# Performance work log

Measured on AMD Instinct MI355X. Metric: run time of the kernel, lower is better.

The kernel has to match this reference:

```python
import jax, jax.numpy as jnp
import numpy as np

NEG_NUM = -10000.0


def setup_inputs() -> dict:
    key = jax.random.key(0)
    k1, k2, k3 = jax.random.split(key, 3)
    B, S, T, D = 8, 4096, 512, 1024
    ctx = jax.random.normal(k1, (B, S, D), dtype=jnp.float32)
    query = jax.random.normal(k2, (B, T, D), dtype=jnp.float32)
    mask = jax.random.randint(k3, (B, S), 0, 2, dtype=jnp.int32)
    return {"ctx": ctx, "query": query, "mask": mask}


def reference(ctx, query, mask):
    # ctx: [B, S, D], query: [B, T, D], mask: [B, S] (0 = masked)
    D = query.shape[-1]
    denom = jnp.asarray(np.sqrt(D), dtype=ctx.dtype)
    # scores[b, t, s] = sum_d query[b, t, d] * ctx[b, s, d]
    scores = jnp.einsum("btd,bsd->bts", query, ctx) / denom
    # apply mask per source position (broadcast over target dim)
    scores = jnp.where(mask[:, None, :] == 0, NEG_NUM, scores)
    p_ctx = jax.nn.softmax(scores, axis=-1)  # [B, T, S]
    expected_ctx = jnp.einsum("bts,bsd->btd", p_ctx, ctx)  # [B, T, D]
    return expected_ctx, p_ctx
```

## Files before the change

### kernel.cpp

```cpp
#include <hip/hip_runtime.h>

#define BB 8
#define SS 4096
#define TT 512
#define DD 1024

typedef __attribute__((ext_vector_type(8))) short bf16x8;
typedef __attribute__((ext_vector_type(4))) short bf16x4;
typedef __attribute__((ext_vector_type(4))) float f32x4;

#define GLOAD_LDS16(gp, lp)                                            \
  __builtin_amdgcn_global_load_lds(                                    \
      (const __attribute__((address_space(1))) void*)(gp),             \
      (__attribute__((address_space(3))) void*)(lp), 16, 0, 0)

__device__ inline unsigned short f2bf(float f) {
  unsigned int u = __float_as_uint(f);
  u += 0x7FFFu + ((u >> 16) & 1u);
  return (unsigned short)(u >> 16);
}
__device__ inline void pack16(const float* __restrict__ src, short* __restrict__ dst) {
  f32x4 f0 = *(const f32x4*)(src + 0);
  f32x4 f1 = *(const f32x4*)(src + 4);
  f32x4 f2 = *(const f32x4*)(src + 8);
  f32x4 f3 = *(const f32x4*)(src + 12);
  bf16x8 b0, b1;
  b0[0] = (short)f2bf(f0.x); b0[1] = (short)f2bf(f0.y);
  b0[2] = (short)f2bf(f0.z); b0[3] = (short)f2bf(f0.w);
  b0[4] = (short)f2bf(f1.x); b0[5] = (short)f2bf(f1.y);
  b0[6] = (short)f2bf(f1.z); b0[7] = (short)f2bf(f1.w);
  b1[0] = (short)f2bf(f2.x); b1[1] = (short)f2bf(f2.y);
  b1[2] = (short)f2bf(f2.z); b1[3] = (short)f2bf(f2.w);
  b1[4] = (short)f2bf(f3.x); b1[5] = (short)f2bf(f3.y);
  b1[6] = (short)f2bf(f3.z); b1[7] = (short)f2bf(f3.w);
  *(bf16x8*)(dst + 0) = b0;
  *(bf16x8*)(dst + 8) = b1;
}

#define WS_NEED ((size_t)168 << 20)
#define OFF_QB  ((size_t)0)
#define OFF_CB  ((size_t)8 << 20)
#define OFF_CT  ((size_t)72 << 20)
#define OFF_PB  ((size_t)136 << 20)
#define OFF_PART ((size_t)0)

__global__ __launch_bounds__(256) void prep_q_kernel(const float* __restrict__ q,
                                                     short* __restrict__ qb) {
  const size_t idx = ((size_t)blockIdx.x * 256 + threadIdx.x) * 16;
  pack16(q + idx, qb + idx);
}

__global__ __launch_bounds__(256) void prep_c_kernel(const float* __restrict__ c,
                                                     short* __restrict__ cb,
                                                     short* __restrict__ ct) {
  const int b  = blockIdx.z;
  const int s0 = blockIdx.y * 64;
  const int d0 = blockIdx.x * 64;
  const float* C = c + (size_t)b * SS * DD;
  __shared__ float Tt[64][65];

  const int tid = threadIdx.x;
#pragma unroll
  for (int h = 0; h < 4; ++h) {
    const int sl = (tid >> 4) + h * 16;
    const int dl = (tid & 15) * 4;
    f32x4 v = *(const f32x4*)(C + (size_t)(s0 + sl) * DD + d0 + dl);
    *(f32x4*)&Tt[sl][dl] = v;
    bf16x4 o;
    o[0] = (short)f2bf(v.x); o[1] = (short)f2bf(v.y);
    o[2] = (short)f2bf(v.z); o[3] = (short)f2bf(v.w);
    *(bf16x4*)(cb + (size_t)b * SS * DD + (size_t)(s0 + sl) * DD + d0 + dl) = o;
  }
  __syncthreads();
#pragma unroll
  for (int g = 0; g < 2; ++g) {
    const int dl = (tid >> 3) + g * 32;
    const int sb = (tid & 7) * 8;
    bf16x8 o;
#pragma unroll
    for (int j = 0; j < 8; ++j) o[j] = (short)f2bf(Tt[sb + j][dl]);
    *(bf16x8*)(ct + (size_t)b * DD * SS + (size_t)(d0 + dl) * SS + s0 + sb) = o;
  }
}


__global__ __launch_bounds__(256) void qk_kernel_f(const short* __restrict__ qb,
                                                   const short* __restrict__ cb,
                                                   const int* __restrict__ mask,
                                                   float* __restrict__ p) {
  const int b  = blockIdx.z;
  const int m0 = blockIdx.y * 128;
  const int n0 = blockIdx.x * 128;
  const short* A  = qb + (size_t)b * TT * DD;
  const short* Bt = cb + (size_t)b * SS * DD;

  __shared__ alignas(16) short As[128 * 64];
  __shared__ alignas(16) short Bs[128 * 64];

  const int tid  = threadIdx.x;
  const int wave = tid >> 6, lane = tid & 63;
  const int quad = lane >> 4, l16 = lane & 15;
  const int wm = (wave >> 1) * 64, wn = (wave & 1) * 64;

  const int rl = lane >> 3;
  const int ck = (lane & 7) ^ (lane >> 3);
  const int x7 = l16 & 7;

  f32x4 acc[4][4];
#pragma unroll
  for (int i = 0; i < 4; ++i)
#pragma unroll
    for (int j = 0; j < 4; ++j) acc[i][j] = (f32x4){0.f, 0.f, 0.f, 0.f};

  for (int k0 = 0; k0 < DD; k0 += 64) {
    __syncthreads();
#pragma unroll
    for (int t = 0; t < 4; ++t) {
      const int rb = wave * 32 + t * 8;
      GLOAD_LDS16(A  + (size_t)(m0 + rb + rl) * DD + k0 + ck * 8, &As[rb * 64]);
      GLOAD_LDS16(Bt + (size_t)(n0 + rb + rl) * DD + k0 + ck * 8, &Bs[rb * 64]);
    }
    __syncthreads();

#pragma unroll
    for (int kk = 0; kk < 2; ++kk) {
      bf16x8 af[4], bfv[4];
#pragma unroll
      for (int i = 0; i < 4; ++i)
        af[i] = *(const bf16x8*)&As[(wm + i * 16 + l16) * 64 +
                                    (((kk * 4 + quad) ^ x7) * 8)];
#pragma unroll
      for (int j = 0; j < 4; ++j)
        bfv[j] = *(const bf16x8*)&Bs[(wn + j * 16 + l16) * 64 +
                                     (((kk * 4 + quad) ^ x7) * 8)];
#pragma unroll
      for (int i = 0; i < 4; ++i)
#pragma unroll
        for (int j = 0; j < 4; ++j)
          acc[i][j] = __builtin_amdgcn_mfma_f32_16x16x32_bf16(af[i], bfv[j],
                                                              acc[i][j], 0, 0, 0);
    }
  }

  float* P = p + (size_t)b * TT * SS;
  int mk[4];
#pragma unroll
  for (int j = 0; j < 4; ++j) mk[j] = mask[b * SS + n0 + wn + j * 16 + l16];
#pragma unroll
  for (int i = 0; i < 4; ++i)
#pragma unroll
    for (int j = 0; j < 4; ++j)
#pragma unroll
      for (int r = 0; r < 4; ++r) {
        const int row = m0 + wm + i * 16 + quad * 4 + r;
        const int col = n0 + wn + j * 16 + l16;
        const float val = (mk[j] == 0) ? -10000.0f : acc[i][j][r] * 0.03125f;
        P[(size_t)row * SS + col] = val;
      }
}

__global__ __launch_bounds__(256) void softmax_kernel_f(float* __restrict__ p,
                                                        short* __restrict__ pb) {
  const int wave = threadIdx.x >> 6, lane = threadIdx.x & 63;
  const int row = blockIdx.x * 4 + wave;
  float* pr = p + (size_t)row * SS;
  short* pbr = pb + (size_t)row * SS;

  f32x4 v[16];
  float mx = -3.0e38f;
#pragma unroll
  for (int h = 0; h < 16; ++h) {
    v[h] = *(const f32x4*)(pr + h * 256 + lane * 4);
    mx = fmaxf(mx, fmaxf(fmaxf(v[h].x, v[h].y), fmaxf(v[h].z, v[h].w)));
  }
#pragma unroll
  for (int off = 32; off > 0; off >>= 1) mx = fmaxf(mx, __shfl_xor(mx, off));

  float sum = 0.f;
#pragma unroll
  for (int h = 0; h < 16; ++h) {
    v[h].x = __expf(v[h].x - mx);
    v[h].y = __expf(v[h].y - mx);
    v[h].z = __expf(v[h].z - mx);
    v[h].w = __expf(v[h].w - mx);
    sum += (v[h].x + v[h].y) + (v[h].z + v[h].w);
  }
#pragma unroll
  for (int off = 32; off > 0; off >>= 1) sum += __shfl_xor(sum, off);
  const float inv = 1.0f / sum;

#pragma unroll
  for (int h = 0; h < 16; ++h) {
    f32x4 o;
    o.x = v[h].x * inv; o.y = v[h].y * inv;
    o.z = v[h].z * inv; o.w = v[h].w * inv;
    *(f32x4*)(pr + h * 256 + lane * 4) = o;
    bf16x4 ob;
    ob[0] = (short)f2bf(o.x); ob[1] = (short)f2bf(o.y);
    ob[2] = (short)f2bf(o.z); ob[3] = (short)f2bf(o.w);
    *(bf16x4*)(pbr + h * 256 + lane * 4) = ob;
  }
}

__global__ __launch_bounds__(256) void pv_kernel_f(const short* __restrict__ pb,
                                                   const short* __restrict__ ct,
                                                   float* __restrict__ part) {
  const int n0 = blockIdx.x * 128;
  const int m0 = blockIdx.y * 128;
  const int z  = blockIdx.z;
  const int b  = z >> 1;
  const int ks = z & 1;
  const short* A  = pb + (size_t)b * TT * SS;
  const short* Bt = ct + (size_t)b * DD * SS;

  __shared__ alignas(16) short As[128 * 64];
  __shared__ alignas(16) short Bs[128 * 64];

  const int tid  = threadIdx.x;
  const int wave = tid >> 6, lane = tid & 63;
  const int quad = lane >> 4, l16 = lane & 15;
  const int wm = (wave >> 1) * 64, wn = (wave & 1) * 64;

  const int rl = lane >> 3;
  const int ck = (lane & 7) ^ (lane >> 3);
  const int x7 = l16 & 7;

  f32x4 acc[4][4];
#pragma unroll
  for (int i = 0; i < 4; ++i)
#pragma unroll
    for (int j = 0; j < 4; ++j) acc[i][j] = (f32x4){0.f, 0.f, 0.f, 0.f};

  const int kend = ks * 2048 + 2048;
  for (int k0 = ks * 2048; k0 < kend; k0 += 64) {
    __syncthreads();
#pragma unroll
    for (int t = 0; t < 4; ++t) {
      const int rb = wave * 32 + t * 8;
      GLOAD_LDS16(A  + (size_t)(m0 + rb + rl) * SS + k0 + ck * 8, &As[rb * 64]);
      GLOAD_LDS16(Bt + (size_t)(n0 + rb + rl) * SS + k0 + ck * 8, &Bs[rb * 64]);
    }
    __syncthreads();

#pragma unroll
    for (int kk = 0; kk < 2; ++kk) {
      bf16x8 af[4], bfv[4];
#pragma unroll
      for (int i = 0; i < 4; ++i)
        af[i] = *(const bf16x8*)&As[(wm + i * 16 + l16) * 64 +
                                    (((kk * 4 + quad) ^ x7) * 8)];
#pragma unroll
      for (int j = 0; j < 4; ++j)
        bfv[j] = *(const bf16x8*)&Bs[(wn + j * 16 + l16) * 64 +
                                     (((kk * 4 + quad) ^ x7) * 8)];
#pragma unroll
      for (int i = 0; i < 4; ++i)
#pragma unroll
        for (int j = 0; j < 4; ++j)
          acc[i][j] = __builtin_amdgcn_mfma_f32_16x16x32_bf16(af[i], bfv[j],
                                                              acc[i][j], 0, 0, 0);
    }
  }

  float* E = part + (size_t)ks * BB * TT * DD + (size_t)b * TT * DD;
#pragma unroll
  for (int i = 0; i < 4; ++i)
#pragma unroll
    for (int j = 0; j < 4; ++j)
#pragma unroll
      for (int r = 0; r < 4; ++r) {
        const int row = m0 + wm + i * 16 + quad * 4 + r;
        const int col = n0 + wn + j * 16 + l16;
        E[(size_t)row * DD + col] = acc[i][j][r];
      }
}

__global__ __launch_bounds__(256) void reduce_kernel(const float* __restrict__ part,
                                                     float* __restrict__ e) {
  const size_t idx = ((size_t)blockIdx.x * 256 + threadIdx.x) * 4;
  const size_t N = (size_t)BB * TT * DD;
  f32x4 a0 = *(const f32x4*)(part + idx);
  f32x4 a1 = *(const f32x4*)(part + N + idx);
  f32x4 o;
  o.x = a0.x + a1.x;
  o.y = a0.y + a1.y;
  o.z = a0.z + a1.z;
  o.w = a0.w + a1.w;
  *(f32x4*)(e + idx) = o;
}

__global__ __launch_bounds__(256) void qk_kernel(const float* __restrict__ q,
                                                 const float* __restrict__ c,
                                                 float* __restrict__ p) {
  const int b  = blockIdx.z;
  const int m0 = blockIdx.y * 128;
  const int n0 = blockIdx.x * 128;
  const float* A  = q + (size_t)b * TT * DD;
  const float* Bt = c + (size_t)b * SS * DD;
  __shared__ alignas(16) short As[128 * 40];
  __shared__ alignas(16) short Bs[128 * 40];
  const int tid  = threadIdx.x;
  const int wave = tid >> 6, lane = tid & 63;
  const int quad = lane >> 4, l16 = lane & 15;
  const int wm = (wave >> 1) * 64, wn = (wave & 1) * 64;
  f32x4 acc[4][4];
#pragma unroll
  for (int i = 0; i < 4; ++i)
#pragma unroll
    for (int j = 0; j < 4; ++j) acc[i][j] = (f32x4){0.f, 0.f, 0.f, 0.f};
  const int ar = tid >> 1;
  const int ak = (tid & 1) * 16;
  for (int k0 = 0; k0 < DD; k0 += 32) {
    __syncthreads();
    pack16(A  + (size_t)(m0 + ar) * DD + k0 + ak, &As[ar * 40 + ak]);
    pack16(Bt + (size_t)(n0 + ar) * DD + k0 + ak, &Bs[ar * 40 + ak]);
    __syncthreads();
    bf16x8 af[4], bfv[4];
#pragma unroll
  for (int i = 0; i < 4; ++i)
      af[i] = *(const bf16x8*)&As[(wm + i * 16 + l16) * 40 + quad * 8];
#pragma unroll
    for (int j = 0; j < 4; ++j)
      bfv[j] = *(const bf16x8*)&Bs[(wn + j * 16 + l16) * 40 + quad * 8];
#pragma unroll
    for (int i = 0; i < 4; ++i)
#pragma unroll
      for (int j = 0; j < 4; ++j)
        acc[i][j] = __builtin_amdgcn_mfma_f32_16x16x32_bf16(af[i], bfv[j],
                                                            acc[i][j], 0, 0, 0);
  }
  float* P = p + (size_t)b * TT * SS;
#pragma unroll
  for (int i = 0; i < 4; ++i)
#pragma unroll
    for (int j = 0; j < 4; ++j)
#pragma unroll
      for (int r = 0; r < 4; ++r) {
        const int row = m0 + wm + i * 16 + quad * 4 + r;
        const int col = n0 + wn + j * 16 + l16;
        P[(size_t)row * SS + col] = acc[i][j][r] * 0.03125f;
      }
}

__global__ __launch_bounds__(256) void softmax_kernel(float* __restrict__ p,
                                                      const int* __restrict__ mask) {
  const int row = blockIdx.x;
  const int b   = row >> 9;
  float* pr = p + (size_t)row * SS;
  const int* mr = mask + b * SS;
  const int tid = threadIdx.x;
  const int wave = tid >> 6, lane = tid & 63;
  float v[16];
  float mx = -3.0e38f;
#pragma unroll
  for (int h = 0; h < 4; ++h) {
    const int base = tid * 4 + h * 1024;
    f32x4 s = *(const f32x4*)(pr + base);
    const int4 m4 = *(const int4*)(mr + base);
#pragma unroll
    for (int j = 0; j < 4; ++j) {
      float f = (j == 0 ? s.x : j == 1 ? s.y : j == 2 ? s.z : s.w);
      const int mk = (j == 0 ? m4.x : j == 1 ? m4.y : j == 2 ? m4.z : m4.w);
      f = fminf(fmaxf(f, -1.0e30f), 1.0e30f);
      f = (mk == 0) ? -10000.0f : f;
      v[h * 4 + j] = f;
      mx = fmaxf(mx, f);
    }
  }
#pragma unroll
  for (int off = 32; off > 0; off >>= 1) mx = fmaxf(mx, __shfl_down(mx, off));
  __shared__ float red[4];
  if (lane == 0) red[wave] = mx;
  __syncthreads();
  mx = fmaxf(fmaxf(red[0], red[1]), fmaxf(red[2], red[3]));
  __syncthreads();
  float e[16];
  float sum = 0.f;
#pragma unroll
  for (int k = 0; k < 16; ++k) { e[k] = __expf(v[k] - mx); sum += e[k]; }
#pragma unroll
  for (int off = 32; off > 0; off >>= 1) sum += __shfl_down(sum, off);
  if (lane == 0) red[wave] = sum;
  __syncthreads();
  const float inv = 1.0f / (red[0] + red[1] + red[2] + red[3]);
#pragma unroll
  for (int h = 0; h < 4; ++h) {
    const int base = tid * 4 + h * 1024;
    f32x4 o;
    o.x = e[h * 4 + 0] * inv; o.y = e[h * 4 + 1] * inv;
    o.z = e[h * 4 + 2] * inv; o.w = e[h * 4 + 3] * inv;
    *(f32x4*)(pr + base) = o;
  }
}

__global__ __launch_bounds__(256) void pv_kernel(const float* __restrict__ p,
                                                 const float* __restrict__ c,
                                                 float* __restrict__ e) {
  const int b  = blockIdx.z;
  const int m0 = blockIdx.y * 128;
  const int n0 = blockIdx.x * 128;
  const float* A  = p + (size_t)b * TT * SS;
  const float* Bm = c + (size_t)b * SS * DD;
  __shared__ alignas(16) short As[128 * 40];
  __shared__ alignas(16) short Bs[128 * 40];
  const int tid  = threadIdx.x;
  const int wave = tid >> 6, lane = tid & 63;
  const int quad = lane >> 4, l16 = lane & 15;
  const int wm = (wave >> 1) * 64, wn = (wave & 1) * 64;
  f32x4 acc[4][4];
#pragma unroll
  for (int i = 0; i < 4; ++i)
#pragma unroll
    for (int j = 0; j < 4; ++j) acc[i][j] = (f32x4){0.f, 0.f, 0.f, 0.f};
  const int ar = tid >> 1;
  const int ak = (tid & 1) * 16;
  const int kk = tid >> 3;
  const int c0 = (tid & 7) * 16;
  for (int k0 = 0; k0 < SS; k0 += 32) {
    __syncthreads();
    pack16(A + (size_t)(m0 + ar) * SS + k0 + ak, &As[ar * 40 + ak]);
    {
      const float* bp = Bm + (size_t)(k0 + kk) * DD + n0 + c0;
#pragma unroll
      for (int h = 0; h < 4; ++h) {
        f32x4 f = *(const f32x4*)(bp + h * 4);
        Bs[(c0 + h * 4 + 0) * 40 + kk] = (short)f2bf(f.x);
        Bs[(c0 + h * 4 + 1) * 40 + kk] = (short)f2bf(f.y);
        Bs[(c0 + h * 4 + 2) * 40 + kk] = (short)f2bf(f.z);
        Bs[(c0 + h * 4 + 3) * 40 + kk] = (short)f2bf(f.w);
      }
    }
    __syncthreads();
    bf16x8 af[4], bfv[4];
#pragma unroll
    for (int i = 0; i < 4; ++i)
      af[i] = *(const bf16x8*)&As[(wm + i * 16 + l16) * 40 + quad * 8];
#pragma unroll
    for (int j = 0; j < 4; ++j)
      bfv[j] = *(const bf16x8*)&Bs[(wn + j * 16 + l16) * 40 + quad * 8];
#pragma unroll
    for (int i = 0; i < 4; ++i)
#pragma unroll
      for (int j = 0; j < 4; ++j)
        acc[i][j] = __builtin_amdgcn_mfma_f32_16x16x32_bf16(af[i], bfv[j],
                                                            acc[i][j], 0, 0, 0);
  }
  float* E = e + (size_t)b * TT * DD;
#pragma unroll
  for (int i = 0; i < 4; ++i)
#pragma unroll
    for (int j = 0; j < 4; ++j)
#pragma unroll
      for (int r = 0; r < 4; ++r) {
        const int row = m0 + wm + i * 16 + quad * 4 + r;
        const int col = n0 + wn + j * 16 + l16;
        E[(size_t)row * DD + col] = acc[i][j][r];
      }
}

extern "C" void kernel_launch(void* const* d_in, const int* in_sizes, int n_in,
                              void* d_out, int out_size, void* d_ws, size_t ws_size,
                              hipStream_t stream) {
  const float* ctx   = (const float*)d_in[0];
  const float* query = (const float*)d_in[1];
  const int*   mask  = (const int*)d_in[2];

  float* expected = (float*)d_out;
  float* p        = (float*)d_out + (size_t)BB * TT * DD;

  if (ws_size >= WS_NEED) {
    char* ws = (char*)d_ws;
    short* qb = (short*)(ws + OFF_QB);
    short* cb = (short*)(ws + OFF_CB);
    short* ct = (short*)(ws + OFF_CT);
    short* pb = (short*)(ws + OFF_PB);
    float* part = (float*)(ws + OFF_PART);

    prep_q_kernel<<<dim3((BB * TT * DD) / (256 * 16)), 256, 0, stream>>>(query, qb);
    prep_c_kernel<<<dim3(DD / 64, SS / 64, BB), 256, 0, stream>>>(ctx, cb, ct);
    qk_kernel_f<<<dim3(SS / 128, TT / 128, BB), 256, 0, stream>>>(qb, cb, mask, p);
    softmax_kernel_f<<<dim3((BB * TT) / 4), 256, 0, stream>>>(p, pb);
    pv_kernel_f<<<dim3(DD / 128, TT / 128, BB * 2), 256, 0, stream>>>(pb, ct, part);
    reduce_kernel<<<dim3((BB * TT * DD) / (256 * 4)), 256, 0, stream>>>(part, expected);
  } else {
    qk_kernel<<<dim3(SS / 128, TT / 128, BB), 256, 0, stream>>>(query, ctx, p);
    softmax_kernel<<<dim3(BB * TT), 256, 0, stream>>>(p, mask);
    pv_kernel<<<dim3(DD / 128, TT / 128, BB), 256, 0, stream>>>(p, ctx, expected);
  }
}
```

Baseline: 398.9 us.

## Double-buffer LDS tiles in QK and PV GEMMs and retile context transpose

The QK and PV GEMM kernels now use two LDS buffers so the async global-to-LDS load of the next K tile is issued before computing on the current tile, leaving one barrier per iteration instead of two. The context prep kernel processes 128 source rows per block, holds all eight loads in registers before converting, and uses an XOR-swizzled float tile for the transpose instead of a padded array. The goal is to hide global load latency behind MFMA work and cut barrier stalls. The cost is doubled LDS per block (64 KB), which may reduce occupancy. The single barrier per iteration may also be insufficient to guarantee the async loads are visible before they are read.

```diff
diff --git a/kernel.cpp b/kernel.cpp
--- a/kernel.cpp
+++ b/kernel.cpp
@@ -54,32 +54,43 @@
                                                      short* __restrict__ cb,
                                                      short* __restrict__ ct) {
   const int b  = blockIdx.z;
-  const int s0 = blockIdx.y * 64;
+  const int s0 = blockIdx.y * 128;
   const int d0 = blockIdx.x * 64;
   const float* C = c + (size_t)b * SS * DD;
-  __shared__ float Tt[64][65];
+  __shared__ float T[128 * 64];
 
   const int tid = threadIdx.x;
-#pragma unroll
-  for (int h = 0; h < 4; ++h) {
-    const int sl = (tid >> 4) + h * 16;
-    const int dl = (tid & 15) * 4;
-    f32x4 v = *(const f32x4*)(C + (size_t)(s0 + sl) * DD + d0 + dl);
-    *(f32x4*)&Tt[sl][dl] = v;
+  const int r0 = tid >> 4;
+  const int cc = tid & 15;
+
+  f32x4 v[8];
+#pragma unroll
+  for (int i = 0; i < 8; ++i)
+    v[i] = *(const f32x4*)(C + (size_t)(s0 + r0 + i * 16) * DD + d0 + cc * 4);
+
+#pragma unroll
+  for (int i = 0; i < 8; ++i) {
+    const int r = r0 + i * 16;
     bf16x4 o;
-    o[0] = (short)f2bf(v.x); o[1] = (short)f2bf(v.y);
-    o[2] = (short)f2bf(v.z); o[3] = (short)f2bf(v.w);
-    *(bf16x4*)(cb + (size_t)b * SS * DD + (size_t)(s0 + sl) * DD + d0 + dl) = o;
+    o[0] = (short)f2bf(v[i].x); o[1] = (short)f2bf(v[i].y);
+    o[2] = (short)f2bf(v[i].z); o[3] = (short)f2bf(v[i].w);
+    *(bf16x4*)(cb + (size_t)b * SS * DD + (size_t)(s0 + r) * DD + d0 + cc * 4) = o;
+    *(f32x4*)&T[r * 64 + ((cc ^ (r >> 3)) & 15) * 4] = v[i];
   }
   __syncthreads();
-#pragma unroll
-  for (int g = 0; g < 2; ++g) {
-    const int dl = (tid >> 3) + g * 32;
-    const int sb = (tid & 7) * 8;
+
+  const int sc  = (tid & 15) * 8;
+  const int dr0 = tid >> 4;
+#pragma unroll
+  for (int i = 0; i < 4; ++i) {
+    const int d = dr0 + i * 16;
     bf16x8 o;
 #pragma unroll
-    for (int j = 0; j < 8; ++j) o[j] = (short)f2bf(Tt[sb + j][dl]);
-    *(bf16x8*)(ct + (size_t)b * DD * SS + (size_t)(d0 + dl) * SS + s0 + sb) = o;
+    for (int j = 0; j < 8; ++j) {
+      const int s = sc + j;
+      o[j] = (short)f2bf(T[s * 64 + (((d >> 2) ^ (s >> 3)) & 15) * 4 + (d & 3)]);
+    }
+    *(bf16x8*)(ct + (size_t)b * DD * SS + (size_t)(d0 + d) * SS + s0 + sc) = o;
   }
 }
 
@@ -94,8 +105,8 @@
   const short* A  = qb + (size_t)b * TT * DD;
   const short* Bt = cb + (size_t)b * SS * DD;
 
-  __shared__ alignas(16) short As[128 * 64];
-  __shared__ alignas(16) short Bs[128 * 64];
+  __shared__ alignas(16) short As[2][128 * 64];
+  __shared__ alignas(16) short Bs[2][128 * 64];
 
   const int tid  = threadIdx.x;
   const int wave = tid >> 6, lane = tid & 63;
@@ -112,35 +123,50 @@
 #pragma unroll
     for (int j = 0; j < 4; ++j) acc[i][j] = (f32x4){0.f, 0.f, 0.f, 0.f};
 
-  for (int k0 = 0; k0 < DD; k0 += 64) {
+#define QK_STAGE(buf, k0)                                                     \
+  {                                                                           \
+    _Pragma("unroll")                                                         \
+    for (int t = 0; t < 4; ++t) {                                             \
+      const int rb = wave * 32 + t * 8;                                       \
+      GLOAD_LDS16(A  + (size_t)(m0 + rb + rl) * DD + (k0) + ck * 8,           \
+                  &As[buf][rb * 64]);                                         \
+      GLOAD_LDS16(Bt + (size_t)(n0 + rb + rl) * DD + (k0) + ck * 8,           \
+                  &Bs[buf][rb * 64]);                                         \
+    }                                                                         \
+  }
+
+#define QK_COMPUTE(buf)                                                       \
+  {                                                                           \
+    _Pragma("unroll")                                                         \
+    for (int kk = 0; kk < 2; ++kk) {                                          \
+      bf16x8 af[4], bfv[4];                                                   \
+      _Pragma("unroll")                                                       \
+      for (int i = 0; i < 4; ++i)                                             \
+        af[i] = *(const bf16x8*)&As[buf][(wm + i * 16 + l16) * 64 +           \
+                                        (((kk * 4 + quad) ^ x7) * 8)];        \
+      _Pragma("unroll")                                                       \
+      for (int j = 0; j < 4; ++j)                                             \
+        bfv[j] = *(const bf16x8*)&Bs[buf][(wn + j * 16 + l16) * 64 +          \
+                                          (((kk * 4 + quad) ^ x7) * 8)];      \
+      _Pragma("unroll")                                                       \
+      for (int i = 0; i < 4; ++i)                                             \
+        _Pragma("unroll")                                                     \
+        for (int j = 0; j < 4; ++j)                                           \
+          acc[i][j] = __builtin_amdgcn_mfma_f32_16x16x32_bf16(                \
+              af[i], bfv[j], acc[i][j], 0, 0, 0);                             \
+    }                                                                         \
+  }
+
+  QK_STAGE(0, 0);
+  __syncthreads();
+  int cur = 0;
+  for (int k0 = 64; k0 < DD; k0 += 64) {
+    QK_STAGE(cur ^ 1, k0);
+    QK_COMPUTE(cur);
     __syncthreads();
-#pragma unroll
-    for (int t = 0; t < 4; ++t) {
-      const int rb = wave * 32 + t * 8;
-      GLOAD_LDS16(A  + (size_t)(m0 + rb + rl) * DD + k0 + ck * 8, &As[rb * 64]);
-      GLOAD_LDS16(Bt + (size_t)(n0 + rb + rl) * DD + k0 + ck * 8, &Bs[rb * 64]);
-    }
-    __syncthreads();
-
-#pragma unroll
-    for (int kk = 0; kk < 2; ++kk) {
-      bf16x8 af[4], bfv[4];
-#pragma unroll
-      for (int i = 0; i < 4; ++i)
-        af[i] = *(const bf16x8*)&As[(wm + i * 16 + l16) * 64 +
-                                    (((kk * 4 + quad) ^ x7) * 8)];
-#pragma unroll
-      for (int j = 0; j < 4; ++j)
-        bfv[j] = *(const bf16x8*)&Bs[(wn + j * 16 + l16) * 64 +
-                                     (((kk * 4 + quad) ^ x7) * 8)];
-#pragma unroll
-      for (int i = 0; i < 4; ++i)
-#pragma unroll
-        for (int j = 0; j < 4; ++j)
-          acc[i][j] = __builtin_amdgcn_mfma_f32_16x16x32_bf16(af[i], bfv[j],
-                                                              acc[i][j], 0, 0, 0);
-    }
-  }
+    cur ^= 1;
+  }
+  QK_COMPUTE(cur);
 
   float* P = p + (size_t)b * TT * SS;
   int mk[4];
@@ -213,8 +239,8 @@
   const short* A  = pb + (size_t)b * TT * SS;
   const short* Bt = ct + (size_t)b * DD * SS;
 
-  __shared__ alignas(16) short As[128 * 64];
-  __shared__ alignas(16) short Bs[128 * 64];
+  __shared__ alignas(16) short As[2][128 * 64];
+  __shared__ alignas(16) short Bs[2][128 * 64];
 
   const int tid  = threadIdx.x;
   const int wave = tid >> 6, lane = tid & 63;
@@ -231,36 +257,30 @@
 #pragma unroll
     for (int j = 0; j < 4; ++j) acc[i][j] = (f32x4){0.f, 0.f, 0.f, 0.f};
 
-  const int kend = ks * 2048 + 2048;
-  for (int k0 = ks * 2048; k0 < kend; k0 += 64) {
+#define PV_STAGE(buf, k0)                                                     \
+  {                                                                           \
+    _Pragma("unroll")                                                         \
+    for (int t = 0; t < 4; ++t) {                                             \
+      const int rb = wave * 32 + t * 8;                                       \
+      GLOAD_LDS16(A  + (size_t)(m0 + rb + rl) * SS + (k0) + ck * 8,           \
+                  &As[buf][rb * 64]);                                         \
+      GLOAD_LDS16(Bt + (size_t)(n0 + rb + rl) * SS + (k0) + ck * 8,           \
+                  &Bs[buf][rb * 64]);                                         \
+    }                                                                         \
+  }
+
+  const int kbeg = ks * 2048;
+  const int kend = kbeg + 2048;
+  PV_STAGE(0, kbeg);
+  __syncthreads();
+  int cur = 0;
+  for (int k0 = kbeg + 64; k0 < kend; k0 += 64) {
+    PV_STAGE(cur ^ 1, k0);
+    QK_COMPUTE(cur);
     __syncthreads();
-#pragma unroll
-    for (int t = 0; t < 4; ++t) {
-      const int rb = wave * 32 + t * 8;
-      GLOAD_LDS16(A  + (size_t)(m0 + rb + rl) * SS + k0 + ck * 8, &As[rb * 64]);
-      GLOAD_LDS16(Bt + (size_t)(n0 + rb + rl) * SS + k0 + ck * 8, &Bs[rb * 64]);
-    }
-    __syncthreads();
-
-#pragma unroll
-    for (int kk = 0; kk < 2; ++kk) {
-      bf16x8 af[4], bfv[4];
-#pragma unroll
-      for (int i = 0; i < 4; ++i)
-        af[i] = *(const bf16x8*)&As[(wm + i * 16 + l16) * 64 +
-                                    (((kk * 4 + quad) ^ x7) * 8)];
-#pragma unroll
-      for (int j = 0; j < 4; ++j)
-        bfv[j] = *(const bf16x8*)&Bs[(wn + j * 16 + l16) * 64 +
-                                     (((kk * 4 + quad) ^ x7) * 8)];
-#pragma unroll
-      for (int i = 0; i < 4; ++i)
-#pragma unroll
-        for (int j = 0; j < 4; ++j)
-          acc[i][j] = __builtin_amdgcn_mfma_f32_16x16x32_bf16(af[i], bfv[j],
-                                                              acc[i][j], 0, 0, 0);
-    }
-  }
+    cur ^= 1;
+  }
+  QK_COMPUTE(cur);
 
   float* E = part + (size_t)ks * BB * TT * DD + (size_t)b * TT * DD;
 #pragma unroll
@@ -477,7 +497,7 @@
     float* part = (float*)(ws + OFF_PART);
 
     prep_q_kernel<<<dim3((BB * TT * DD) / (256 * 16)), 256, 0, stream>>>(query, qb);
-    prep_c_kernel<<<dim3(DD / 64, SS / 64, BB), 256, 0, stream>>>(ctx, cb, ct);
+    prep_c_kernel<<<dim3(DD / 64, SS / 128, BB), 256, 0, stream>>>(ctx, cb, ct);
     qk_kernel_f<<<dim3(SS / 128, TT / 128, BB), 256, 0, stream>>>(qb, cb, mask, p);
     softmax_kernel_f<<<dim3((BB * TT) / 4), 256, 0, stream>>>(p, pb);
     pv_kernel_f<<<dim3(DD / 128, TT / 128, BB * 2), 256, 0, stream>>>(pb, ct, part);
```

Result: no change. 399.3 us (+0.1%).
